# Performance work log

Measured on AMD Instinct MI355X. Metric: run time of the kernel, lower is better.

## Reference

```python
import jax, jax.numpy as jnp
import numpy as np

K = 3  # kernel size
PAD = 1
STRIDE = 1


def conv3x3(x, w, b):
    # x: [B,C,H,W], w: [O,I,3,3], b: [O]
    y = jax.lax.conv_general_dilated(
        x, w, window_strides=(STRIDE, STRIDE), padding=[(PAD, PAD), (PAD, PAD)],
        dimension_numbers=("NCHW", "OIHW", "NCHW"))
    return y + b[None, :, None, None]


def deform_conv2d(x, offsets, w, b):
    # x: [B,C,H,W]; offsets: [B,2*K*K,H,W] layout (dy,dx) per kernel tap;
    # w: [O,C,K,K]; b: [O]. stride=1, pad=1, dilation=1 (matches module).
    B, C, H, W = x.shape
    K2 = K * K
    off = offsets.reshape(B, K2, 2, H, W)
    dy, dx = off[:, :, 0], off[:, :, 1]  # [B,K2,H,W]

    ki, kj = jnp.meshgrid(jnp.arange(K), jnp.arange(K), indexing="ij")
    rel_y = (ki - PAD).reshape(K2).astype(x.dtype)  # kernel tap offsets
    rel_x = (kj - PAD).reshape(K2).astype(x.dtype)
    hh = jnp.arange(H, dtype=x.dtype)
    ww = jnp.arange(W, dtype=x.dtype)

    # sampling positions [B,K2,H,W]
    py = hh[None, None, :, None] + rel_y[None, :, None, None] + dy
    px = ww[None, None, None, :] + rel_x[None, :, None, None] + dx

    y0 = jnp.floor(py)
    x0 = jnp.floor(px)
    wy = py - y0  # bilinear weights
    wx = px - x0
    y0i = y0.astype(jnp.int32)
    x0i = x0.astype(jnp.int32)

    xf = x.reshape(B, C, H * W)

    def gather(yi, xi):
        valid = ((yi >= 0) & (yi < H) & (xi >= 0) & (xi < W)).astype(x.dtype)
        yc = jnp.clip(yi, 0, H - 1)
        xc = jnp.clip(xi, 0, W - 1)
        idx = (yc * W + xc).reshape(B, 1, K2 * H * W)
        v = jnp.take_along_axis(xf, idx, axis=2).reshape(B, C, K2, H, W)
        return v * valid.reshape(B, 1, K2, H, W)

    w00 = ((1 - wy) * (1 - wx))[:, None]  # [B,1,K2,H,W]
    w01 = ((1 - wy) * wx)[:, None]
    w10 = (wy * (1 - wx))[:, None]
    w11 = (wy * wx)[:, None]

    val = (w00 * gather(y0i, x0i) + w01 * gather(y0i, x0i + 1)
           + w10 * gather(y0i + 1, x0i) + w11 * gather(y0i + 1, x0i + 1))
    # accumulate over channels and kernel taps
    out = jnp.einsum("ock,bckhw->bohw", w.reshape(w.shape[0], C, K2), val)
    return out + b[None, :, None, None]


def setup_inputs() -> dict:
    key = jax.random.key(0)
    k1, k2, k3, k4 = jax.random.split(key, 4)
    B, Cin, Cout, H, W = 4, 256, 256, 80, 80
    x = jax.random.normal(k1, (B, Cin, H, W), dtype=jnp.float32)
    # offset-predicting conv: small init so predicted offsets are modest
    offset_w = jax.random.normal(k2, (2 * K * K, Cin, 3, 3), dtype=jnp.float32) * 0.01
    offset_b = jnp.zeros((2 * K * K,), dtype=jnp.float32)
    conv_w = jax.random.normal(k3, (Cout, Cin, K, K), dtype=jnp.float32) * (1.0 / np.sqrt(Cin * K * K))
    conv_b = jax.random.normal(k4, (Cout,), dtype=jnp.float32) * 0.01
    return {"x": x, "offset_w": offset_w, "offset_b": offset_b,
            "conv_w": conv_w, "conv_b": conv_b}


def reference(x, offset_w, offset_b, conv_w, conv_b):
    offsets = conv3x3(x, offset_w, offset_b)
    return deform_conv2d(x, offsets, conv_w, conv_b)
```

## Files before the change

### kernel.cpp

```cpp
#include <hip/hip_runtime.h>

#define CB 4
#define CIN 256
#define COUT 256
#define HH 80
#define WW 80
#define HW (HH*WW)
#define K2 9
#define NKC 72
#define LDSROW 56

typedef unsigned short ushort_t;
typedef __attribute__((ext_vector_type(8))) short bf16x8;
typedef __attribute__((ext_vector_type(4))) float f32x4;

__device__ __forceinline__ ushort_t f2bf(float f) {
    unsigned int b = __float_as_uint(f);
    b += 0x7fffu + ((b >> 16) & 1u);
    return (ushort_t)(b >> 16);
}
__device__ __forceinline__ float bflo(unsigned int u) { return __uint_as_float(u << 16); }
__device__ __forceinline__ float bfhi(unsigned int u) { return __uint_as_float(u & 0xffff0000u); }

__device__ __forceinline__ unsigned int blendpack(unsigned int a, unsigned int b,
                                                  unsigned int c, unsigned int d,
                                                  float w0, float w1, float w2, float w3) {
    float lo = w0*bflo(a) + w1*bflo(b) + w2*bflo(c) + w3*bflo(d);
    float hi = w0*bfhi(a) + w1*bfhi(b) + w2*bfhi(c) + w3*bfhi(d);
    unsigned int r;
    asm("v_cvt_pk_bf16_f32 %0, %1, %2" : "=v"(r) : "v"(lo), "v"(hi));
    return r;
}

__global__ __launch_bounds__(256) void transpose_x(const float* __restrict__ x,
                                                   ushort_t* __restrict__ xb) {
    __shared__ ushort_t tile[64*256];
    const int b = blockIdx.x / (HW/64);
    const int hw0 = (blockIdx.x % (HW/64)) * 64;
    const int tid = threadIdx.x;
    const int px4 = (tid & 15) * 4;
    const int cb0 = tid >> 4;
    const float* xp = x + (size_t)b*CIN*HW + hw0 + px4;
    #pragma unroll
    for (int p = 0; p < 16; ++p) {
        const int c = cb0 * 16 + p;
        const float4 v = *(const float4*)(xp + (size_t)c*HW);
        const int blk = c >> 3, sub = c & 7;
        tile[(px4+0)*256 + (((blk) ^ ((px4+0)&31))<<3) + sub] = f2bf(v.x);
        tile[(px4+1)*256 + (((blk) ^ ((px4+1)&31))<<3) + sub] = f2bf(v.y);
        tile[(px4+2)*256 + (((blk) ^ ((px4+2)&31))<<3) + sub] = f2bf(v.z);
        tile[(px4+3)*256 + (((blk) ^ ((px4+3)&31))<<3) + sub] = f2bf(v.w);
    }
    __syncthreads();
    const int g = tid & 31;
    #pragma unroll
    for (int p = 0; p < 8; ++p) {
        const int px = (tid >> 5) + p*8;
        const uint4 r = *(const uint4*)&tile[px*256 + ((g ^ (px&31))<<3)];
        *(uint4*)&xb[((size_t)b*HW + hw0 + px)*CIN + g*8] = r;
    }
}

__global__ __launch_bounds__(256) void pack_w(const float* __restrict__ conv_w,
                                              const float* __restrict__ offset_w,
                                              ushort_t* __restrict__ wmain,
                                              ushort_t* __restrict__ woff) {
    const int t = blockIdx.x * 256 + threadIdx.x;
    if (t < NKC*16*64) {
        const int kc = t >> 10;
        const int mt = (t >> 6) & 15;
        const int l  = t & 63;
        const int m  = mt*16 + (l & 15);
        const int kb = kc*32 + ((l >> 4) << 3);
        ushort_t v[8];
        #pragma unroll
        for (int i = 0; i < 8; ++i) {
            const int kg = kb + i;
            const int tap = kg >> 8;
            const int c = kg & 255;
            v[i] = f2bf(conv_w[(size_t)(m*CIN + c)*K2 + tap]);
        }
        uint4 r;
        r.x = v[0] | ((unsigned)v[1] << 16);
        r.y = v[2] | ((unsigned)v[3] << 16);
        r.z = v[4] | ((unsigned)v[5] << 16);
        r.w = v[6] | ((unsigned)v[7] << 16);
        *(uint4*)&wmain[(size_t)t*8] = r;
    } else if (t < NKC*16*64 + NKC*2*64) {
        const int t2 = t - NKC*16*64;
        const int kc = t2 >> 7;
        const int mt = (t2 >> 6) & 1;
        const int l  = t2 & 63;
        const int m  = mt*16 + (l & 15);
        const int kb = kc*32 + ((l >> 4) << 3);
        ushort_t v[8];
        #pragma unroll
        for (int i = 0; i < 8; ++i) {
            const int kg = kb + i;
            const int tap = kg >> 8;
            const int c = kg & 255;
            v[i] = (m < 18) ? f2bf(offset_w[(size_t)(m*CIN + c)*K2 + tap]) : (ushort_t)0;
        }
        uint4 r;
        r.x = v[0] | ((unsigned)v[1] << 16);
        r.y = v[2] | ((unsigned)v[3] << 16);
        r.z = v[4] | ((unsigned)v[5] << 16);
        r.w = v[6] | ((unsigned)v[7] << 16);
        *(uint4*)&woff[(size_t)t2*8] = r;
    }
}

__global__ __launch_bounds__(256) void deform_main(const ushort_t* __restrict__ xb,
                                                   const ushort_t* __restrict__ wmain,
                                                   const ushort_t* __restrict__ woff,
                                                   const float* __restrict__ offset_b,
                                                   const float* __restrict__ conv_b,
                                                   float* __restrict__ out) {
    __shared__ ushort_t ldsB[2][64*LDSROW];
    __shared__ float off_lds[18][64];
    __shared__ float bw[K2][64][4];
    __shared__ int   bi[K2][64][4];

    const int tid = threadIdx.x;
    const int lane = tid & 63;
    const int wv = tid >> 6;
    const int bid = blockIdx.x;
    const int bb = bid / (HW/64);
    const int hwb = (bid % (HW/64)) * 64;
    const ushort_t* xbase = xb + (size_t)bb * HW * CIN;
    const int px = tid >> 2, cg = tid & 3;

    {
        const int mt = wv >> 1;
        const int nt0 = (wv & 1) * 2;
        f32x4 a0 = {0.f,0.f,0.f,0.f}, a1 = {0.f,0.f,0.f,0.f};
        const int hw = hwb + px;
        const int ph = hw / WW, pw = hw - ph*WW;

        uint4 v;
        {
            const int yy = ph - 1, xx = pw - 1;
            v = make_uint4(0u,0u,0u,0u);
            if (yy >= 0 && yy < HH && xx >= 0 && xx < WW)
                v = *(const uint4*)(xbase + (yy*WW + xx)*CIN + cg*8);
        }
        for (int kc = 0; kc < NKC; ++kc) {
            const bf16x8 af = *(const bf16x8*)(woff + ((size_t)(kc*2 + mt)*64 + lane)*8);
            *(uint4*)&ldsB[kc&1][px*LDSROW + cg*8] = v;
            if (kc+1 < NKC) {
                const int tap = (kc+1) >> 3;
                const int c0 = ((kc+1) & 7)*32 + cg*8;
                const int yy = ph + tap/3 - 1;
                const int xx = pw + tap%3 - 1;
                uint4 nv = make_uint4(0u,0u,0u,0u);
                if (yy >= 0 && yy < HH && xx >= 0 && xx < WW)
                    nv = *(const uint4*)(xbase + (yy*WW + xx)*CIN + c0);
                v = nv;
            }
            asm volatile("s_waitcnt lgkmcnt(0)" ::: "memory");
            __builtin_amdgcn_s_barrier();
            const bf16x8 bf0 = *(const bf16x8*)&ldsB[kc&1][(nt0*16 + (lane&15))*LDSROW + (lane>>4)*8];
            const bf16x8 bf1 = *(const bf16x8*)&ldsB[kc&1][((nt0+1)*16 + (lane&15))*LDSROW + (lane>>4)*8];
            a0 = __builtin_amdgcn_mfma_f32_16x16x32_bf16(af, bf0, a0, 0, 0, 0);
            a1 = __builtin_amdgcn_mfma_f32_16x16x32_bf16(af, bf1, a1, 0, 0, 0);
        }
        const int r0 = (lane >> 4) * 4;
        #pragma unroll
        for (int j = 0; j < 4; ++j) {
            const int oc = mt*16 + r0 + j;
            if (oc < 18) {
                const float ob = offset_b[oc];
                off_lds[oc][nt0*16 + (lane & 15)]     = a0[j] + ob;
                off_lds[oc][(nt0+1)*16 + (lane & 15)] = a1[j] + ob;
            }
        }
    }
    __syncthreads();

    for (int it = tid; it < K2*64; it += 256) {
        const int tap = it >> 6, pxl = it & 63;
        const int hw = hwb + pxl;
        const int ph = hw / WW, pw = hw - ph*WW;
        const float dy = off_lds[tap*2][pxl];
        const float dx = off_lds[tap*2 + 1][pxl];
        const float py  = (float)(ph + tap/3 - 1) + dy;
        const float pxx = (float)(pw + tap%3 - 1) + dx;
        const float y0f = floorf(py), x0f = floorf(pxx);
        const float wy = py - y0f, wx = pxx - x0f;
        const int y0 = (int)y0f, x0 = (int)x0f;
        const int y1 = y0 + 1, x1 = x0 + 1;
        const float vy0 = (y0 >= 0 && y0 < HH) ? 1.f : 0.f;
        const float vy1 = (y1 >= 0 && y1 < HH) ? 1.f : 0.f;
        const float vx0 = (x0 >= 0 && x0 < WW) ? 1.f : 0.f;
        const float vx1 = (x1 >= 0 && x1 < WW) ? 1.f : 0.f;
        const int y0c = min(max(y0, 0), HH-1), y1c = min(max(y1, 0), HH-1);
        const int x0c = min(max(x0, 0), WW-1), x1c = min(max(x1, 0), WW-1);
        bw[tap][pxl][0] = (1.f-wy)*(1.f-wx)*vy0*vx0;
        bw[tap][pxl][1] = (1.f-wy)*wx*vy0*vx1;
        bw[tap][pxl][2] = wy*(1.f-wx)*vy1*vx0;
        bw[tap][pxl][3] = wy*wx*vy1*vx1;
        bi[tap][pxl][0] = (y0c*WW + x0c)*CIN;
        bi[tap][pxl][1] = (y0c*WW + x1c)*CIN;
        bi[tap][pxl][2] = (y1c*WW + x0c)*CIN;
        bi[tap][pxl][3] = (y1c*WW + x1c)*CIN;
    }
    __syncthreads();

    f32x4 acc[4][4];
    #pragma unroll
    for (int mi = 0; mi < 4; ++mi)
        #pragma unroll
        for (int ni = 0; ni < 4; ++ni)
            acc[mi][ni] = (f32x4){0.f,0.f,0.f,0.f};

    const int mt0 = wv * 4;
    float4 wt;
    uint4 ca, cbv, ccv, cdv;
    {
        wt = *(const float4*)bw[0][px];
        const int4 ix = *(const int4*)bi[0][px];
        const int c0 = cg*8;
        ca  = *(const uint4*)(xbase + ix.x + c0);
        cbv = *(const uint4*)(xbase + ix.y + c0);
        ccv = *(const uint4*)(xbase + ix.z + c0);
        cdv = *(const uint4*)(xbase + ix.w + c0);
    }

    #pragma unroll 2
    for (int kc = 0; kc < NKC; ++kc) {
        bf16x8 afr[4];
        #pragma unroll
        for (int mi = 0; mi < 4; ++mi)
            afr[mi] = *(const bf16x8*)(wmain + ((size_t)(kc*16 + mt0 + mi)*64 + lane)*8);
        uint4 r;
        r.x = blendpack(ca.x, cbv.x, ccv.x, cdv.x, wt.x, wt.y, wt.z, wt.w);
        r.y = blendpack(ca.y, cbv.y, ccv.y, cdv.y, wt.x, wt.y, wt.z, wt.w);
        r.z = blendpack(ca.z, cbv.z, ccv.z, cdv.z, wt.x, wt.y, wt.z, wt.w);
        r.w = blendpack(ca.w, cbv.w, ccv.w, cdv.w, wt.x, wt.y, wt.z, wt.w);
        *(uint4*)&ldsB[kc&1][px*LDSROW + cg*8] = r;
        if (kc+1 < NKC) {
            const int tapn = (kc+1) >> 3;
            const int c0n = ((kc+1) & 7)*32 + cg*8;
            const float4 wtn = *(const float4*)bw[tapn][px];
            const int4 ixn = *(const int4*)bi[tapn][px];
            ca  = *(const uint4*)(xbase + ixn.x + c0n);
            cbv = *(const uint4*)(xbase + ixn.y + c0n);
            ccv = *(const uint4*)(xbase + ixn.z + c0n);
            cdv = *(const uint4*)(xbase + ixn.w + c0n);
            wt = wtn;
        }
        asm volatile("s_waitcnt lgkmcnt(0)" ::: "memory");
        __builtin_amdgcn_s_barrier();
        bf16x8 bfr[4];
        #pragma unroll
        for (int ni = 0; ni < 4; ++ni)
            bfr[ni] = *(const bf16x8*)&ldsB[kc&1][(ni*16 + (lane&15))*LDSROW + (lane>>4)*8];
        #pragma unroll
        for (int mi = 0; mi < 4; ++mi)
            #pragma unroll
            for (int ni = 0; ni < 4; ++ni)
                acc[mi][ni] = __builtin_amdgcn_mfma_f32_16x16x32_bf16(afr[mi], bfr[ni], acc[mi][ni], 0, 0, 0);
    }

    #pragma unroll
    for (int mi = 0; mi < 4; ++mi) {
        #pragma unroll
        for (int ni = 0; ni < 4; ++ni) {
            const int pxl = ni*16 + (lane & 15);
            #pragma unroll
            for (int j = 0; j < 4; ++j) {
                const int o = (mt0 + mi)*16 + (lane >> 4)*4 + j;
                out[((size_t)bb*COUT + o)*HW + hwb + pxl] = acc[mi][ni][j] + conv_b[o];
            }
        }
    }
}

extern "C" void kernel_launch(void* const* d_in, const int* in_sizes, int n_in,
                              void* d_out, int out_size, void* d_ws, size_t ws_size,
                              hipStream_t stream) {
    const float* x        = (const float*)d_in[0];
    const float* offset_w = (const float*)d_in[1];
    const float* offset_b = (const float*)d_in[2];
    const float* conv_w   = (const float*)d_in[3];
    const float* conv_b   = (const float*)d_in[4];
    float* out = (float*)d_out;

    char* wsb = (char*)d_ws;
    ushort_t* xb    = (ushort_t*)wsb;
    ushort_t* wmain = (ushort_t*)(wsb + (size_t)CB*HW*CIN*2);
    ushort_t* woff  = (ushort_t*)(wsb + (size_t)CB*HW*CIN*2 + (size_t)NKC*16*64*8*2);

    hipLaunchKernelGGL(transpose_x, dim3(CB*(HW/64)), dim3(256), 0, stream, x, xb);
    hipLaunchKernelGGL(pack_w, dim3(324), dim3(256), 0, stream, conv_w, offset_w, wmain, woff);
    hipLaunchKernelGGL(deform_main, dim3(CB*(HW/64)), dim3(256), 0, stream,
                       xb, wmain, woff, offset_b, conv_b, out);
}
```

Before: 178.0 us.

## Deepen deform-conv gather pipeline, drop offset-phase barriers, fuse prep kernels

The main GEMM loop now runs a two-stage register pipeline. Bilinear-corner gathers are issued two K-chunks ahead and the A-fragment weights one chunk ahead, to hide global gather latency behind MFMA work. The offset-prediction phase gives each wave a private LDS slice covering 32 pixels, which removes the per-chunk block barriers but duplicates some global loads across waves. The transpose and weight-pack kernels are merged into one launch, and block indices are remapped to group neighbouring strips for cache locality. The cost is higher register pressure and redundant phase-1 loads.

```diff
diff --git a/kernel.cpp b/kernel.cpp
--- a/kernel.cpp
+++ b/kernel.cpp
@@ -9,6 +9,8 @@
 #define K2 9
 #define NKC 72
 #define LDSROW 56
+#define NSTRIP (HW/64)
+#define NBLK (CB*NSTRIP)
 
 typedef unsigned short ushort_t;
 typedef __attribute__((ext_vector_type(8))) short bf16x8;
@@ -32,82 +34,130 @@
     return r;
 }
 
-__global__ __launch_bounds__(256) void transpose_x(const float* __restrict__ x,
-                                                   ushort_t* __restrict__ xb) {
+__global__ __launch_bounds__(256) void prep(const float* __restrict__ x,
+                                            const float* __restrict__ conv_w,
+                                            const float* __restrict__ offset_w,
+                                            ushort_t* __restrict__ xb,
+                                            ushort_t* __restrict__ wmain,
+                                            ushort_t* __restrict__ woff) {
     __shared__ ushort_t tile[64*256];
-    const int b = blockIdx.x / (HW/64);
-    const int hw0 = (blockIdx.x % (HW/64)) * 64;
     const int tid = threadIdx.x;
-    const int px4 = (tid & 15) * 4;
-    const int cb0 = tid >> 4;
-    const float* xp = x + (size_t)b*CIN*HW + hw0 + px4;
+    if (blockIdx.x < NBLK) {
+        const int b = blockIdx.x / NSTRIP;
+        const int hw0 = (blockIdx.x % NSTRIP) * 64;
+        const int px4 = (tid & 15) * 4;
+        const int cb0 = tid >> 4;
+        const float* xp = x + (size_t)b*CIN*HW + hw0 + px4;
+        #pragma unroll
+        for (int p = 0; p < 16; ++p) {
+            const int c = cb0 * 16 + p;
+            const float4 v = *(const float4*)(xp + (size_t)c*HW);
+            const int blk = c >> 3, sub = c & 7;
+            tile[(px4+0)*256 + (((blk) ^ ((px4+0)&31))<<3) + sub] = f2bf(v.x);
+            tile[(px4+1)*256 + (((blk) ^ ((px4+1)&31))<<3) + sub] = f2bf(v.y);
+            tile[(px4+2)*256 + (((blk) ^ ((px4+2)&31))<<3) + sub] = f2bf(v.z);
+            tile[(px4+3)*256 + (((blk) ^ ((px4+3)&31))<<3) + sub] = f2bf(v.w);
+        }
+        __syncthreads();
+        const int g = tid & 31;
+        #pragma unroll
+        for (int p = 0; p < 8; ++p) {
+            const int px = (tid >> 5) + p*8;
+            const uint4 r = *(const uint4*)&tile[px*256 + ((g ^ (px&31))<<3)];
+            *(uint4*)&xb[((size_t)b*HW + hw0 + px)*CIN + g*8] = r;
+        }
+    } else {
+        const int t = (blockIdx.x - NBLK) * 256 + tid;
+        if (t < NKC*16*64) {
+            const int kc = t >> 10;
+            const int mt = (t >> 6) & 15;
+            const int l  = t & 63;
+            const int m  = mt*16 + (l & 15);
+            const int kb = kc*32 + ((l >> 4) << 3);
+            ushort_t v[8];
+            #pragma unroll
+            for (int i = 0; i < 8; ++i) {
+                const int kg = kb + i;
+                const int tap = kg >> 8;
+                const int c = kg & 255;
+                v[i] = f2bf(conv_w[(size_t)(m*CIN + c)*K2 + tap]);
+            }
+            uint4 r;
+            r.x = v[0] | ((unsigned)v[1] << 16);
+            r.y = v[2] | ((unsigned)v[3] << 16);
+            r.z = v[4] | ((unsigned)v[5] << 16);
+            r.w = v[6] | ((unsigned)v[7] << 16);
+            *(uint4*)&wmain[(size_t)t*8] = r;
+        } else if (t < NKC*16*64 + NKC*2*64) {
+            const int t2 = t - NKC*16*64;
+            const int kc = t2 >> 7;
+            const int mt = (t2 >> 6) & 1;
+            const int l  = t2 & 63;
+            const int m  = mt*16 + (l & 15);
+            const int kb = kc*32 + ((l >> 4) << 3);
+            ushort_t v[8];
+            #pragma unroll
+            for (int i = 0; i < 8; ++i) {
+                const int kg = kb + i;
+                const int tap = kg >> 8;
+                const int c = kg & 255;
+                v[i] = (m < 18) ? f2bf(offset_w[(size_t)(m*CIN + c)*K2 + tap]) : (ushort_t)0;
+            }
+            uint4 r;
+            r.x = v[0] | ((unsigned)v[1] << 16);
+            r.y = v[2] | ((unsigned)v[3] << 16);
+            r.z = v[4] | ((unsigned)v[5] << 16);
+            r.w = v[6] | ((unsigned)v[7] << 16);
+            *(uint4*)&woff[(size_t)t2*8] = r;
+        }
+    }
+}
+
+template<int BUF>
+__device__ __forceinline__ void p3step(int kc, const ushort_t* __restrict__ xbase,
+                                       const ushort_t* __restrict__ wmain,
+                                       ushort_t* __restrict__ ldsB,
+                                       const float (&bw)[K2][64][4], const int (&bi)[K2][64][4],
+                                       uint4 &A0, uint4 &A1, uint4 &A2, uint4 &A3, float4 &wtA,
+                                       bf16x8 (&afU)[4], bf16x8 (&afI)[4], f32x4 (&acc)[4][4],
+                                       int pxg, int cg, int lane, int mt0) {
+    float4 wtT; int4 ixT;
+    const bool have = (kc + 2) < NKC;
+    if (have) {
+        const int tapT = (kc + 2) >> 3;
+        wtT = *(const float4*)bw[tapT][pxg];
+        ixT = *(const int4*)bi[tapT][pxg];
+    }
+    if (kc + 1 < NKC) {
+        #pragma unroll
+        for (int mi = 0; mi < 4; ++mi)
+            afI[mi] = *(const bf16x8*)(wmain + ((size_t)((kc+1)*16 + mt0 + mi)*64 + lane)*8);
+    }
+    uint4 r;
+    r.x = blendpack(A0.x, A1.x, A2.x, A3.x, wtA.x, wtA.y, wtA.z, wtA.w);
+    r.y = blendpack(A0.y, A1.y, A2.y, A3.y, wtA.x, wtA.y, wtA.z, wtA.w);
+    r.z = blendpack(A0.z, A1.z, A2.z, A3.z, wtA.x, wtA.y, wtA.z, wtA.w);
+    r.w = blendpack(A0.w, A1.w, A2.w, A3.w, wtA.x, wtA.y, wtA.z, wtA.w);
+    *(uint4*)&ldsB[BUF*64*LDSROW + pxg*LDSROW + cg*8] = r;
+    if (have) {
+        const int c0n = ((kc+2) & 7)*32 + cg*8;
+        A0 = *(const uint4*)(xbase + ixT.x + c0n);
+        A1 = *(const uint4*)(xbase + ixT.y + c0n);
+        A2 = *(const uint4*)(xbase + ixT.z + c0n);
+        A3 = *(const uint4*)(xbase + ixT.w + c0n);
+        wtA = wtT;
+    }
+    asm volatile("s_waitcnt lgkmcnt(0)" ::: "memory");
+    __builtin_amdgcn_s_barrier();
+    bf16x8 bfr[4];
     #pragma unroll
-    for (int p = 0; p < 16; ++p) {
-        const int c = cb0 * 16 + p;
-        const float4 v = *(const float4*)(xp + (size_t)c*HW);
-        const int blk = c >> 3, sub = c & 7;
-        tile[(px4+0)*256 + (((blk) ^ ((px4+0)&31))<<3) + sub] = f2bf(v.x);
-        tile[(px4+1)*256 + (((blk) ^ ((px4+1)&31))<<3) + sub] = f2bf(v.y);
-        tile[(px4+2)*256 + (((blk) ^ ((px4+2)&31))<<3) + sub] = f2bf(v.z);
-        tile[(px4+3)*256 + (((blk) ^ ((px4+3)&31))<<3) + sub] = f2bf(v.w);
-    }
-    __syncthreads();
-    const int g = tid & 31;
+    for (int ni = 0; ni < 4; ++ni)
+        bfr[ni] = *(const bf16x8*)&ldsB[BUF*64*LDSROW + (ni*16 + (lane&15))*LDSROW + (lane>>4)*8];
     #pragma unroll
-    for (int p = 0; p < 8; ++p) {
-        const int px = (tid >> 5) + p*8;
-        const uint4 r = *(const uint4*)&tile[px*256 + ((g ^ (px&31))<<3)];
-        *(uint4*)&xb[((size_t)b*HW + hw0 + px)*CIN + g*8] = r;
-    }
-}
-
-__global__ __launch_bounds__(256) void pack_w(const float* __restrict__ conv_w,
-                                              const float* __restrict__ offset_w,
-                                              ushort_t* __restrict__ wmain,
-                                              ushort_t* __restrict__ woff) {
-    const int t = blockIdx.x * 256 + threadIdx.x;
-    if (t < NKC*16*64) {
-        const int kc = t >> 10;
-        const int mt = (t >> 6) & 15;
-        const int l  = t & 63;
-        const int m  = mt*16 + (l & 15);
-        const int kb = kc*32 + ((l >> 4) << 3);
-        ushort_t v[8];
-        #pragma unroll
-        for (int i = 0; i < 8; ++i) {
-            const int kg = kb + i;
-            const int tap = kg >> 8;
-            const int c = kg & 255;
-            v[i] = f2bf(conv_w[(size_t)(m*CIN + c)*K2 + tap]);
-        }
-        uint4 r;
-        r.x = v[0] | ((unsigned)v[1] << 16);
-        r.y = v[2] | ((unsigned)v[3] << 16);
-        r.z = v[4] | ((unsigned)v[5] << 16);
-        r.w = v[6] | ((unsigned)v[7] << 16);
-        *(uint4*)&wmain[(size_t)t*8] = r;
-    } else if (t < NKC*16*64 + NKC*2*64) {
-        const int t2 = t - NKC*16*64;
-        const int kc = t2 >> 7;
-        const int mt = (t2 >> 6) & 1;
-        const int l  = t2 & 63;
-        const int m  = mt*16 + (l & 15);
-        const int kb = kc*32 + ((l >> 4) << 3);
-        ushort_t v[8];
-        #pragma unroll
-        for (int i = 0; i < 8; ++i) {
-            const int kg = kb + i;
-            const int tap = kg >> 8;
-            const int c = kg & 255;
-            v[i] = (m < 18) ? f2bf(offset_w[(size_t)(m*CIN + c)*K2 + tap]) : (ushort_t)0;
-        }
-        uint4 r;
-        r.x = v[0] | ((unsigned)v[1] << 16);
-        r.y = v[2] | ((unsigned)v[3] << 16);
-        r.z = v[4] | ((unsigned)v[5] << 16);
-        r.w = v[6] | ((unsigned)v[7] << 16);
-        *(uint4*)&woff[(size_t)t2*8] = r;
-    }
+    for (int mi = 0; mi < 4; ++mi)
+        #pragma unroll
+        for (int ni = 0; ni < 4; ++ni)
+            acc[mi][ni] = __builtin_amdgcn_mfma_f32_16x16x32_bf16(afU[mi], bfr[ni], acc[mi][ni], 0, 0, 0);
 }
 
 __global__ __launch_bounds__(256) void deform_main(const ushort_t* __restrict__ xb,
@@ -116,7 +166,7 @@
                                                    const float* __restrict__ offset_b,
                                                    const float* __restrict__ conv_b,
                                                    float* __restrict__ out) {
-    __shared__ ushort_t ldsB[2][64*LDSROW];
+    __shared__ __align__(16) char lds_pool[20480];
     __shared__ float off_lds[18][64];
     __shared__ float bw[K2][64][4];
     __shared__ int   bi[K2][64][4];
@@ -124,54 +174,69 @@
     const int tid = threadIdx.x;
     const int lane = tid & 63;
     const int wv = tid >> 6;
-    const int bid = blockIdx.x;
-    const int bb = bid / (HW/64);
-    const int hwb = (bid % (HW/64)) * 64;
+    const int sb = (blockIdx.x & 7) * (NBLK/8) + (blockIdx.x >> 3);
+    const int bb = sb / NSTRIP;
+    const int hwb = (sb % NSTRIP) * 64;
     const ushort_t* xbase = xb + (size_t)bb * HW * CIN;
-    const int px = tid >> 2, cg = tid & 3;
+    const int pxg = tid >> 2, cg = tid & 3;
 
     {
         const int mt = wv >> 1;
-        const int nt0 = (wv & 1) * 2;
+        const int p0 = (wv & 1) * 32;
+        ushort_t* myB = (ushort_t*)lds_pool + wv * 2560;
         f32x4 a0 = {0.f,0.f,0.f,0.f}, a1 = {0.f,0.f,0.f,0.f};
-        const int hw = hwb + px;
+        const int pxl = lane >> 1;
+        const int ch  = lane & 1;
+        const int hw = hwb + p0 + pxl;
         const int ph = hw / WW, pw = hw - ph*WW;
 
-        uint4 v;
-        {
-            const int yy = ph - 1, xx = pw - 1;
-            v = make_uint4(0u,0u,0u,0u);
-            if (yy >= 0 && yy < HH && xx >= 0 && xx < WW)
-                v = *(const uint4*)(xbase + (yy*WW + xx)*CIN + cg*8);
-        }
-        for (int kc = 0; kc < NKC; ++kc) {
-            const bf16x8 af = *(const bf16x8*)(woff + ((size_t)(kc*2 + mt)*64 + lane)*8);
-            *(uint4*)&ldsB[kc&1][px*LDSROW + cg*8] = v;
-            if (kc+1 < NKC) {
-                const int tap = (kc+1) >> 3;
-                const int c0 = ((kc+1) & 7)*32 + cg*8;
-                const int yy = ph + tap/3 - 1;
-                const int xx = pw + tap%3 - 1;
-                uint4 nv = make_uint4(0u,0u,0u,0u);
-                if (yy >= 0 && yy < HH && xx >= 0 && xx < WW)
-                    nv = *(const uint4*)(xbase + (yy*WW + xx)*CIN + c0);
-                v = nv;
-            }
-            asm volatile("s_waitcnt lgkmcnt(0)" ::: "memory");
-            __builtin_amdgcn_s_barrier();
-            const bf16x8 bf0 = *(const bf16x8*)&ldsB[kc&1][(nt0*16 + (lane&15))*LDSROW + (lane>>4)*8];
-            const bf16x8 bf1 = *(const bf16x8*)&ldsB[kc&1][((nt0+1)*16 + (lane&15))*LDSROW + (lane>>4)*8];
-            a0 = __builtin_amdgcn_mfma_f32_16x16x32_bf16(af, bf0, a0, 0, 0, 0);
-            a1 = __builtin_amdgcn_mfma_f32_16x16x32_bf16(af, bf1, a1, 0, 0, 0);
-        }
+        uint4 u0a, u0b, u1a, u1b;
+        #define P1LOAD(UA, UB, KC_) { \
+            const int tap_ = (KC_) >> 3; \
+            const int c0_ = ((KC_) & 7)*32 + ch*16; \
+            const int yy_ = ph + tap_/3 - 1, xx_ = pw + tap_%3 - 1; \
+            UA = make_uint4(0u,0u,0u,0u); UB = make_uint4(0u,0u,0u,0u); \
+            if (yy_ >= 0 && yy_ < HH && xx_ >= 0 && xx_ < WW) { \
+                const ushort_t* p_ = xbase + (yy_*WW + xx_)*CIN + c0_; \
+                UA = *(const uint4*)p_; UB = *(const uint4*)(p_ + 8); } }
+
+        P1LOAD(u0a, u0b, 0);
+        P1LOAD(u1a, u1b, 1);
+        for (int kp = 0; kp < NKC/2; ++kp) {
+            {
+                const int kc = 2*kp;
+                const bf16x8 af = *(const bf16x8*)(woff + ((size_t)(kc*2 + mt)*64 + lane)*8);
+                ushort_t* wb = myB + pxl*40 + ch*16;
+                *(uint4*)wb = u0a;
+                *(uint4*)(wb + 8) = u0b;
+                if (kp + 1 < NKC/2) P1LOAD(u0a, u0b, 2*kp + 2);
+                const bf16x8 b0 = *(const bf16x8*)(myB + (lane&15)*40 + (lane>>4)*8);
+                const bf16x8 b1 = *(const bf16x8*)(myB + (16 + (lane&15))*40 + (lane>>4)*8);
+                a0 = __builtin_amdgcn_mfma_f32_16x16x32_bf16(af, b0, a0, 0, 0, 0);
+                a1 = __builtin_amdgcn_mfma_f32_16x16x32_bf16(af, b1, a1, 0, 0, 0);
+            }
+            {
+                const int kc = 2*kp + 1;
+                const bf16x8 af = *(const bf16x8*)(woff + ((size_t)(kc*2 + mt)*64 + lane)*8);
+                ushort_t* wb = myB + 1280 + pxl*40 + ch*16;
+                *(uint4*)wb = u1a;
+                *(uint4*)(wb + 8) = u1b;
+                if (kp + 1 < NKC/2) P1LOAD(u1a, u1b, 2*kp + 3);
+                const bf16x8 b0 = *(const bf16x8*)(myB + 1280 + (lane&15)*40 + (lane>>4)*8);
+                const bf16x8 b1 = *(const bf16x8*)(myB + 1280 + (16 + (lane&15))*40 + (lane>>4)*8);
+                a0 = __builtin_amdgcn_mfma_f32_16x16x32_bf16(af, b0, a0, 0, 0, 0);
+                a1 = __builtin_amdgcn_mfma_f32_16x16x32_bf16(af, b1, a1, 0, 0, 0);
+            }
+        }
+        #undef P1LOAD
         const int r0 = (lane >> 4) * 4;
         #pragma unroll
         for (int j = 0; j < 4; ++j) {
             const int oc = mt*16 + r0 + j;
             if (oc < 18) {
                 const float ob = offset_b[oc];
-                off_lds[oc][nt0*16 + (lane & 15)]     = a0[j] + ob;
-                off_lds[oc][(nt0+1)*16 + (lane & 15)] = a1[j] + ob;
+                off_lds[oc][p0 + (lane & 15)]      = a0[j] + ob;
+                off_lds[oc][p0 + 16 + (lane & 15)] = a1[j] + ob;
             }
         }
     }
@@ -213,53 +278,33 @@
         for (int ni = 0; ni < 4; ++ni)
             acc[mi][ni] = (f32x4){0.f,0.f,0.f,0.f};
 
+    ushort_t* ldsB = (ushort_t*)lds_pool;
     const int mt0 = wv * 4;
-    float4 wt;
-    uint4 ca, cbv, ccv, cdv;
+    float4 wtA, wtB;
+    uint4 A0, A1, A2, A3, B0, B1, B2, B3;
+    bf16x8 afA[4], afB[4];
     {
-        wt = *(const float4*)bw[0][px];
-        const int4 ix = *(const int4*)bi[0][px];
-        const int c0 = cg*8;
-        ca  = *(const uint4*)(xbase + ix.x + c0);
-        cbv = *(const uint4*)(xbase + ix.y + c0);
-        ccv = *(const uint4*)(xbase + ix.z + c0);
-        cdv = *(const uint4*)(xbase + ix.w + c0);
-    }
-
-    #pragma unroll 2
-    for (int kc = 0; kc < NKC; ++kc) {
-        bf16x8 afr[4];
+        wtA = *(const float4*)bw[0][pxg];
+        const int4 ix0 = *(const int4*)bi[0][pxg];
+        const int c00 = cg*8;
+        A0 = *(const uint4*)(xbase + ix0.x + c00);
+        A1 = *(const uint4*)(xbase + ix0.y + c00);
+        A2 = *(const uint4*)(xbase + ix0.z + c00);
+        A3 = *(const uint4*)(xbase + ix0.w + c00);
+        wtB = *(const float4*)bw[0][pxg];
+        const int4 ix1 = *(const int4*)bi[0][pxg];
+        const int c01 = 32 + cg*8;
+        B0 = *(const uint4*)(xbase + ix1.x + c01);
+        B1 = *(const uint4*)(xbase + ix1.y + c01);
+        B2 = *(const uint4*)(xbase + ix1.z + c01);
+        B3 = *(const uint4*)(xbase + ix1.w + c01);
         #pragma unroll
         for (int mi = 0; mi < 4; ++mi)
-            afr[mi] = *(const bf16x8*)(wmain + ((size_t)(kc*16 + mt0 + mi)*64 + lane)*8);
-        uint4 r;
-        r.x = blendpack(ca.x, cbv.x, ccv.x, cdv.x, wt.x, wt.y, wt.z, wt.w);
-        r.y = blendpack(ca.y, cbv.y, ccv.y, cdv.y, wt.x, wt.y, wt.z, wt.w);
-        r.z = blendpack(ca.z, cbv.z, ccv.z, cdv.z, wt.x, wt.y, wt.z, wt.w);
-        r.w = blendpack(ca.w, cbv.w, ccv.w, cdv.w, wt.x, wt.y, wt.z, wt.w);
-        *(uint4*)&ldsB[kc&1][px*LDSROW + cg*8] = r;
-        if (kc+1 < NKC) {
-            const int tapn = (kc+1) >> 3;
-            const int c0n = ((kc+1) & 7)*32 + cg*8;
-            const float4 wtn = *(const float4*)bw[tapn][px];
-            const int4 ixn = *(const int4*)bi[tapn][px];
-            ca  = *(const uint4*)(xbase + ixn.x + c0n);
-            cbv = *(const uint4*)(xbase + ixn.y + c0n);
-            ccv = *(const uint4*)(xbase + ixn.z + c0n);
-            cdv = *(const uint4*)(xbase + ixn.w + c0n);
-            wt = wtn;
-        }
-        asm volatile("s_waitcnt lgkmcnt(0)" ::: "memory");
-        __builtin_amdgcn_s_barrier();
-        bf16x8 bfr[4];
-        #pragma unroll
-        for (int ni = 0; ni < 4; ++ni)
-            bfr[ni] = *(const bf16x8*)&ldsB[kc&1][(ni*16 + (lane&15))*LDSROW + (lane>>4)*8];
-        #pragma unroll
-        for (int mi = 0; mi < 4; ++mi)
-            #pragma unroll
-            for (int ni = 0; ni < 4; ++ni)
-                acc[mi][ni] = __builtin_amdgcn_mfma_f32_16x16x32_bf16(afr[mi], bfr[ni], acc[mi][ni], 0, 0, 0);
+            afA[mi] = *(const bf16x8*)(wmain + ((size_t)(mt0 + mi)*64 + lane)*8);
+    }
+    for (int kp = 0; kp < NKC/2; ++kp) {
+        p3step<0>(2*kp,     xbase, wmain, ldsB, bw, bi, A0, A1, A2, A3, wtA, afA, afB, acc, pxg, cg, lane, mt0);
+        p3step<1>(2*kp + 1, xbase, wmain, ldsB, bw, bi, B0, B1, B2, B3, wtB, afB, afA, acc, pxg, cg, lane, mt0);
     }
 
     #pragma unroll
@@ -291,8 +336,8 @@
     ushort_t* wmain = (ushort_t*)(wsb + (size_t)CB*HW*CIN*2);
     ushort_t* woff  = (ushort_t*)(wsb + (size_t)CB*HW*CIN*2 + (size_t)NKC*16*64*8*2);
 
-    hipLaunchKernelGGL(transpose_x, dim3(CB*(HW/64)), dim3(256), 0, stream, x, xb);
-    hipLaunchKernelGGL(pack_w, dim3(324), dim3(256), 0, stream, conv_w, offset_w, wmain, woff);
-    hipLaunchKernelGGL(deform_main, dim3(CB*(HW/64)), dim3(256), 0, stream,
+    hipLaunchKernelGGL(prep, dim3(NBLK + 324), dim3(256), 0, stream,
+                       x, conv_w, offset_w, xb, wmain, woff);
+    hipLaunchKernelGGL(deform_main, dim3(NBLK), dim3(256), 0, stream,
                        xb, wmain, woff, offset_b, conv_b, out);
 }
```

Result: faster. 158.0 us (-11.2%).
